# Kernel tuning notes

Hardware: AMD Instinct MI355X
Metric: run time of the kernel (lower is better)

Reference implementation:

```python
import jax, jax.numpy as jnp
import numpy as np

B, C, N, H = 4, 256, 1024, 8
D = C            # per-head q/k dim (out_channels defaults to in_channels)
DV = C           # per-head value/output dim (y_out_channels defaults to out_channels)


def setup_inputs() -> dict:
    key = jax.random.key(0)
    ks = jax.random.split(key, 10)
    s = 0.02
    return {
        "x": jax.random.normal(ks[0], (B, C, N), jnp.float32),
        "y": jax.random.normal(ks[1], (B, C, N), jnp.float32),
        "Wq": jax.random.normal(ks[2], (H * D, C), jnp.float32) * s,
        "bq": jnp.zeros((H * D,), jnp.float32),
        "Wk": jax.random.normal(ks[3], (H * D, C), jnp.float32) * s,
        "bk": jnp.zeros((H * D,), jnp.float32),
        "Wv": jax.random.normal(ks[4], (H * DV, C), jnp.float32) * s,
        "bv": jnp.zeros((H * DV,), jnp.float32),
        "Wp": jax.random.normal(ks[5], (DV, C), jnp.float32) * s,  # projection, bias=False
        "gamma": jax.random.uniform(ks[6], (H, 1, 1, 1), jnp.float32) + 0.001,
    }


def _pconv(t, W, b):
    # 1x1 conv1d: (O,C) x (B,C,N) -> (B,O,N)
    out = jnp.einsum('oc,bcn->bon', W, t)
    return out if b is None else out + b[None, :, None]


def reference(x, y, Wq, bq, Wk, bk, Wv, bv, Wp, gamma):
    b_, _, n_ = x.shape
    h = gamma.shape[0]
    # Q/K/V projections, split channels into h heads (head-major chunks of D)
    q = _pconv(x, Wq, bq).reshape(b_, h, -1, n_)   # [B,H,D,N]
    k = _pconv(x, Wk, bk).reshape(b_, h, -1, n_)   # [B,H,D,N]
    v = _pconv(y, Wv, bv).reshape(b_, h, -1, n_)   # [B,H,DV,N]
    # energy[i,j] = sum_d q[d,i]*k[d,j]; softmax over keys j (no sqrt(d) scaling)
    attn = jax.nn.softmax(jnp.einsum('bhdn,bhdm->bhnm', q, k), axis=-1)
    out = jnp.einsum('bhdm,bhnm->bhdn', v, attn)   # [B,H,DV,N]
    # residual branch: y projected to DV channels (1x1 conv, no bias)
    yp = jnp.einsum('oc,bcn->bon', Wp, y)          # [B,DV,N]
    g = gamma.reshape(1, h, 1, 1)
    out = (g * out + yp[:, None, :, :]) / (1.0 + g)
    # concat heads along channel dim (head-major), matching split_cat(out,1,0,2)
    return out.reshape(b_, -1, n_)                 # [B,H*DV,N]
```

## Files before the change

### kernel.cpp

```cpp
#include <hip/hip_runtime.h>

#define Bb 4
#define Cc 256
#define Nn 1024
#define Hh 8
#define Oo 2048

typedef __attribute__((ext_vector_type(8))) short bf16x8;
typedef __attribute__((ext_vector_type(4))) float f32x4;

__device__ __forceinline__ short f2bf(float f) {
  unsigned u = __builtin_bit_cast(unsigned, f);
  unsigned r = u + 0x7FFFu + ((u >> 16) & 1u);
  return (short)(r >> 16);
}
__device__ __forceinline__ f32x4 mfma16(bf16x8 a, bf16x8 b, f32x4 c) {
  return __builtin_amdgcn_mfma_f32_16x16x32_bf16(a, b, c, 0, 0, 0);
}
__device__ __forceinline__ void gl_lds16(const void* g, void* l) {
  __builtin_amdgcn_global_load_lds(
      (const __attribute__((address_space(1))) void*)g,
      (__attribute__((address_space(3))) void*)l, 16, 0, 0);
}

__device__ __forceinline__ void stage_row512(const char* gbase, char* lds,
                                             int wave, int lane) {
#pragma unroll
  for (int i = 0; i < 8; i++) {
    int off = (wave * 8 + i) * 1024;
    int L = off + lane * 16;
    int r = L >> 9;
    int c = ((L >> 4) & 31) ^ (r & 7);
    gl_lds16(gbase + r * 512 + c * 16, lds + off);
  }
}
__device__ __forceinline__ void stage_v(const char* Vg, char* lds, int k0,
                                        int wave, int lane) {
#pragma unroll
  for (int i = 0; i < 8; i++) {
    int off = (wave * 8 + i) * 1024;
    int L = off + lane * 16;
    int r = L >> 7;
    int c = ((L >> 4) & 7) ^ (r & 7);
    gl_lds16(Vg + (size_t)r * 2048 + k0 * 2 + c * 16, lds + off);
  }
}

__global__ __launch_bounds__(256) void k_transpose(
    const float* __restrict__ x, const float* __restrict__ y,
    short* __restrict__ xT, short* __restrict__ yT,
    const float* __restrict__ Wq, const float* __restrict__ Wk,
    const float* __restrict__ Wv, const float* __restrict__ Wp,
    short* __restrict__ dWq, short* __restrict__ dWk, short* __restrict__ dWv,
    short* __restrict__ dWp) {
  {
    const int NW = Oo * Cc;
    int lin = blockIdx.x + 16 * (blockIdx.y + 4 * blockIdx.z);
    for (int i = (lin * 256 + threadIdx.x) * 4; i < 3 * NW + Cc * Cc;
         i += 512 * 256 * 4) {
      const float* src;
      short* dst;
      int off;
      if (i < NW) {
        src = Wq; dst = dWq; off = i;
      } else if (i < 2 * NW) {
        src = Wk; dst = dWk; off = i - NW;
      } else if (i < 3 * NW) {
        src = Wv; dst = dWv; off = i - 2 * NW;
      } else {
        src = Wp; dst = dWp; off = i - 3 * NW;
      }
      float4 v = *(const float4*)(src + off);
      short4 o;
      o.x = f2bf(v.x);
      o.y = f2bf(v.y);
      o.z = f2bf(v.z);
      o.w = f2bf(v.w);
      *(short4*)(dst + off) = o;
    }
  }
  int bz = blockIdx.z;
  int b = bz >> 1;
  const float* src = (bz & 1) ? y : x;
  short* dst = (bz & 1) ? yT : xT;
  src += (size_t)b * Cc * Nn;
  dst += (size_t)b * Nn * Cc;
  __shared__ short tile[64][68];
  int n0 = blockIdx.x * 64, c0 = blockIdx.y * 64;
  int t = threadIdx.x;
#pragma unroll
  for (int i = 0; i < 4; i++) {
    int idx = t + i * 256;
    int cc = idx >> 4, ng = idx & 15;
    float4 v = *(const float4*)(src + (size_t)(c0 + cc) * Nn + n0 + ng * 4);
    short4 o;
    o.x = f2bf(v.x);
    o.y = f2bf(v.y);
    o.z = f2bf(v.z);
    o.w = f2bf(v.w);
    *(short4*)&tile[cc][ng * 4] = o;
  }
  __syncthreads();
#pragma unroll
  for (int i = 0; i < 4; i++) {
    int idx = t + i * 256;
    int nn = idx >> 4, c4 = idx & 15;
    short4 o;
    o.x = tile[c4 * 4 + 0][nn];
    o.y = tile[c4 * 4 + 1][nn];
    o.z = tile[c4 * 4 + 2][nn];
    o.w = tile[c4 * 4 + 3][nn];
    *(short4*)(dst + (size_t)(n0 + nn) * Cc + c0 + c4 * 4) = o;
  }
}

__global__ __launch_bounds__(256, 4) void k_proj(
    const short* __restrict__ xT, const short* __restrict__ yT,
    const short* __restrict__ Wqb, const float* __restrict__ bq,
    const short* __restrict__ Wkb, const float* __restrict__ bk,
    const short* __restrict__ Wvb, const float* __restrict__ bv,
    const short* __restrict__ Wpb, short* __restrict__ Qt,
    short* __restrict__ Kt, short* __restrict__ Vv, float* __restrict__ yp) {
  int b = blockIdx.z, n0 = blockIdx.x * 64;
  int yb = blockIdx.y;
  int path = yb >> 5;
  int o0 = (yb & 31) * 64;
  const short* W = path == 0 ? Wqb : path == 1 ? Wkb : path == 2 ? Wvb : Wpb;
  bool dataStaged = path >= 2;
  int wave = threadIdx.x >> 6, lane = threadIdx.x & 63;
  int quad = lane >> 4, l16 = lane & 15;
  int sw = l16 & 7;
  __shared__ short Ws[64 * 256];

  const char* stage_src =
      dataStaged ? (const char*)(yT + (size_t)b * Nn * Cc + (size_t)n0 * Cc)
                 : (const char*)(W + (size_t)o0 * Cc);
  stage_row512(stage_src, (char*)Ws, wave, lane);

  const short* aptr =
      dataStaged
          ? W + (size_t)(o0 + wave * 16 + l16) * Cc + quad * 8
          : xT + (size_t)b * Nn * Cc + (size_t)(n0 + wave * 16 + l16) * Cc +
                quad * 8;
  bf16x8 areg[8];
#pragma unroll
  for (int ks = 0; ks < 8; ks++) areg[ks] = *(const bf16x8*)(aptr + ks * 32);

  f32x4 acc[4];
#pragma unroll
  for (int j = 0; j < 4; j++) acc[j] = f32x4{0.f, 0.f, 0.f, 0.f};
  __syncthreads();
#pragma unroll
  for (int ks = 0; ks < 8; ks++) {
#pragma unroll
    for (int cj = 0; cj < 4; cj++) {
      int off = (cj * 16 + l16) * 512 + (((ks * 4 + quad) ^ sw) << 4);
      bf16x8 wf = *(const bf16x8*)((const char*)Ws + off);
      if (dataStaged)
        acc[cj] = mfma16(areg[ks], wf, acc[cj]);
      else
        acc[cj] = mfma16(wf, areg[ks], acc[cj]);
    }
  }
  if (path < 2) {
    short* Od = path == 0 ? Qt : Kt;
    const float* bias = path == 0 ? bq : bk;
#pragma unroll
    for (int cj = 0; cj < 4; cj++) {
      int obase = o0 + cj * 16 + quad * 4;
      int h = obase >> 8, d = obase & 255;
      int n = n0 + wave * 16 + l16;
      float4 vb = *(const float4*)(bias + obase);
      size_t idx = (((size_t)(b * Hh + h) * Nn) + n) * 256 + d;
      short4 o;
      o.x = f2bf(acc[cj][0] + vb.x);
      o.y = f2bf(acc[cj][1] + vb.y);
      o.z = f2bf(acc[cj][2] + vb.z);
      o.w = f2bf(acc[cj][3] + vb.w);
      *(short4*)(Od + idx) = o;
    }
  } else {
#pragma unroll
    for (int cj = 0; cj < 4; cj++) {
      int n = n0 + cj * 16 + l16;
#pragma unroll
      for (int r = 0; r < 4; r++) {
        int o = o0 + wave * 16 + quad * 4 + r;
        if (path == 3) {
          yp[((size_t)b * Cc + o) * Nn + n] = acc[cj][r];
        } else {
          float v = acc[cj][r] + bv[o];
          Vv[((size_t)b * Oo + o) * Nn + n] = f2bf(v);
        }
      }
    }
  }
}

__global__ __launch_bounds__(256) void k_attn(
    const short* __restrict__ Qt, const short* __restrict__ Kt,
    const short* __restrict__ Vv, const float* __restrict__ yp,
    const float* __restrict__ gamma, float* __restrict__ out) {
  int id = blockIdx.x;
  int bh = (id & 7) * 4 + (id >> 7);
  int q0 = ((id >> 3) & 15) * 64;
  int b = bh >> 3, h = bh & 7;
  int wave = threadIdx.x >> 6, lane = threadIdx.x & 63;
  int quad = lane >> 4, l16 = lane & 15;
  int sw = l16 & 7;
  const short* Qb = Qt + (size_t)bh * Nn * 256;
  const char* Kg = (const char*)(Kt + (size_t)bh * Nn * 256);
  const char* Vg = (const char*)(Vv + (size_t)bh * 256 * Nn);

  __shared__ short Klds[64 * 256];
  __shared__ short Vlds[256 * 64];
  __shared__ short plds[4][16][64];
  __shared__ float llds[64];

  bf16x8 qreg[8];
  {
    const short* qp = Qb + (size_t)(q0 + wave * 16 + l16) * 256 + quad * 8;
#pragma unroll
    for (int ks = 0; ks < 8; ks++) qreg[ks] = *(const bf16x8*)(qp + ks * 32);
  }
  f32x4 oacc[16];
#pragma unroll
  for (int j = 0; j < 16; j++) oacc[j] = f32x4{0.f, 0.f, 0.f, 0.f};
  float l_i[4] = {0.f, 0.f, 0.f, 0.f};

  stage_row512(Kg, (char*)Klds, wave, lane);
  stage_v(Vg, (char*)Vlds, 0, wave, lane);

  for (int kt = 0; kt < 16; kt++) {
    int k0 = kt * 64;
    __syncthreads();
    f32x4 sc[4];
#pragma unroll
    for (int j = 0; j < 4; j++) sc[j] = f32x4{0.f, 0.f, 0.f, 0.f};
#pragma unroll
    for (int ks = 0; ks < 8; ks++) {
#pragma unroll
      for (int cj = 0; cj < 4; cj++) {
        bf16x8 kb = *(const bf16x8*)((const char*)Klds +
                                     (cj * 16 + l16) * 512 +
                                     (((ks * 4 + quad) ^ sw) << 4));
        sc[cj] = mfma16(qreg[ks], kb, sc[cj]);
      }
    }
#pragma unroll
    for (int cj = 0; cj < 4; cj++) {
#pragma unroll
      for (int r = 0; r < 4; r++) {
        float p = __expf(sc[cj][r]);
        l_i[r] += p;
        int row = quad * 4 + r;
        plds[wave][row][(((cj * 2 + (l16 >> 3)) ^ (row & 7)) << 3) | sw] =
            f2bf(p);
      }
    }
    __syncthreads();
    if (kt < 15)
      stage_row512(Kg + (size_t)(k0 + 64) * 512, (char*)Klds, wave, lane);
    bf16x8 ap0[4], ap1[4];
#pragma unroll
    for (int qb = 0; qb < 4; qb++) {
      ap0[qb] = *(const bf16x8*)&plds[qb][l16][(quad ^ sw) << 3];
      ap1[qb] = *(const bf16x8*)&plds[qb][l16][((quad + 4) ^ sw) << 3];
    }
#pragma unroll
    for (int dj = 0; dj < 4; dj++) {
      const char* vrow = (const char*)Vlds + (wave * 64 + dj * 16 + l16) * 128;
      bf16x8 v0 = *(const bf16x8*)(vrow + ((quad ^ sw) << 4));
      bf16x8 v1 = *(const bf16x8*)(vrow + (((quad + 4) ^ sw) << 4));
#pragma unroll
      for (int qb = 0; qb < 4; qb++) {
        oacc[qb * 4 + dj] = mfma16(ap0[qb], v0, oacc[qb * 4 + dj]);
        oacc[qb * 4 + dj] = mfma16(ap1[qb], v1, oacc[qb * 4 + dj]);
      }
    }
    __syncthreads();
    if (kt < 15) stage_v(Vg, (char*)Vlds, k0 + 64, wave, lane);
  }
#pragma unroll
  for (int r = 0; r < 4; r++) {
    float v = l_i[r];
    v += __shfl_xor(v, 1);
    v += __shfl_xor(v, 2);
    v += __shfl_xor(v, 4);
    v += __shfl_xor(v, 8);
    l_i[r] = v;
  }
  if (l16 == 0) {
    f32x4 lv;
#pragma unroll
    for (int r = 0; r < 4; r++) lv[r] = l_i[r];
    *(f32x4*)&llds[wave * 16 + quad * 4] = lv;
  }
  __syncthreads();
  float gf = gamma[h];
  float sg = gf / (1.f + gf), sy = 1.f / (1.f + gf);
#pragma unroll
  for (int qb = 0; qb < 4; qb++) {
    f32x4 lv = *(const f32x4*)&llds[qb * 16 + quad * 4];
    int qq = q0 + qb * 16 + quad * 4;
#pragma unroll
    for (int dj = 0; dj < 4; dj++) {
      int dv = wave * 64 + dj * 16 + l16;
      const float* ypp = yp + ((size_t)b * 256 + dv) * Nn + qq;
      float* op = out + ((size_t)b * Oo + h * 256 + dv) * Nn + qq;
      float4 yv = *(const float4*)ypp;
      f32x4 oa = oacc[qb * 4 + dj];
      float4 ov;
      ov.x = sg * (oa[0] / lv[0]) + sy * yv.x;
      ov.y = sg * (oa[1] / lv[1]) + sy * yv.y;
      ov.z = sg * (oa[2] / lv[2]) + sy * yv.z;
      ov.w = sg * (oa[3] / lv[3]) + sy * yv.w;
      *(float4*)op = ov;
    }
  }
}

extern "C" void kernel_launch(void* const* d_in, const int* in_sizes, int n_in,
                              void* d_out, int out_size, void* d_ws,
                              size_t ws_size, hipStream_t stream) {
  const float* x = (const float*)d_in[0];
  const float* y = (const float*)d_in[1];
  const float* Wq = (const float*)d_in[2];
  const float* bq = (const float*)d_in[3];
  const float* Wk = (const float*)d_in[4];
  const float* bk = (const float*)d_in[5];
  const float* Wv = (const float*)d_in[6];
  const float* bv = (const float*)d_in[7];
  const float* Wp = (const float*)d_in[8];
  const float* gamma = (const float*)d_in[9];
  float* out = (float*)d_out;

  char* w = (char*)d_ws;
  short* Qt = (short*)(w + 0);
  short* Kt = (short*)(w + 16777216);
  short* Vv = (short*)(w + 33554432);
  short* xT = (short*)(w + 50331648);
  short* yT = (short*)(w + 52428800);
  float* yp = (float*)(w + 54525952);
  short* Wqb = (short*)(w + 58720256);
  short* Wkb = (short*)(w + 59768832);
  short* Wvb = (short*)(w + 60817408);
  short* Wpb = (short*)(w + 61865984);

  k_transpose<<<dim3(Nn / 64, Cc / 64, 2 * Bb), dim3(256), 0, stream>>>(
      x, y, xT, yT, Wq, Wk, Wv, Wp, Wqb, Wkb, Wvb, Wpb);
  k_proj<<<dim3(Nn / 64, 100, Bb), dim3(256), 0, stream>>>(
      xT, yT, Wqb, bq, Wkb, bk, Wvb, bv, Wpb, Qt, Kt, Vv, yp);
  k_attn<<<dim3(512), dim3(256), 0, stream>>>(Qt, Kt, Vv, yp, gamma, out);
}
```

Before: 189.5 us.

## Split attention block across eight waves partitioning keys and value dims

Result: no change. 192.2 us (+1.4%).

```diff
diff --git a/kernel.cpp b/kernel.cpp
--- a/kernel.cpp
+++ b/kernel.cpp
@@ -34,11 +34,22 @@
     gl_lds16(gbase + r * 512 + c * 16, lds + off);
   }
 }
-__device__ __forceinline__ void stage_v(const char* Vg, char* lds, int k0,
-                                        int wave, int lane) {
-#pragma unroll
-  for (int i = 0; i < 8; i++) {
-    int off = (wave * 8 + i) * 1024;
+__device__ __forceinline__ void stage_row512_8(const char* gbase, char* lds,
+                                               int wave, int lane) {
+#pragma unroll
+  for (int i = 0; i < 4; i++) {
+    int off = (wave * 4 + i) * 1024;
+    int L = off + lane * 16;
+    int r = L >> 9;
+    int c = ((L >> 4) & 31) ^ (r & 7);
+    gl_lds16(gbase + r * 512 + c * 16, lds + off);
+  }
+}
+__device__ __forceinline__ void stage_v8(const char* Vg, char* lds, int k0,
+                                         int wave, int lane) {
+#pragma unroll
+  for (int i = 0; i < 4; i++) {
+    int off = (wave * 4 + i) * 1024;
     int L = off + lane * 16;
     int r = L >> 7;
     int c = ((L >> 4) & 7) ^ (r & 7);
@@ -197,7 +208,7 @@
   }
 }
 
-__global__ __launch_bounds__(256) void k_attn(
+__global__ __launch_bounds__(512, 4) void k_attn(
     const short* __restrict__ Qt, const short* __restrict__ Kt,
     const short* __restrict__ Vv, const float* __restrict__ yp,
     const float* __restrict__ gamma, float* __restrict__ out) {
@@ -206,6 +217,7 @@
   int q0 = ((id >> 3) & 15) * 64;
   int b = bh >> 3, h = bh & 7;
   int wave = threadIdx.x >> 6, lane = threadIdx.x & 63;
+  int wq = wave >> 1, wk = wave & 1;
   int quad = lane >> 4, l16 = lane & 15;
   int sw = l16 & 7;
   const short* Qb = Qt + (size_t)bh * Nn * 256;
@@ -215,71 +227,71 @@
   __shared__ short Klds[64 * 256];
   __shared__ short Vlds[256 * 64];
   __shared__ short plds[4][16][64];
-  __shared__ float llds[64];
+  __shared__ float llds[2][64];
 
   bf16x8 qreg[8];
   {
-    const short* qp = Qb + (size_t)(q0 + wave * 16 + l16) * 256 + quad * 8;
+    const short* qp = Qb + (size_t)(q0 + wq * 16 + l16) * 256 + quad * 8;
 #pragma unroll
     for (int ks = 0; ks < 8; ks++) qreg[ks] = *(const bf16x8*)(qp + ks * 32);
   }
-  f32x4 oacc[16];
-#pragma unroll
-  for (int j = 0; j < 16; j++) oacc[j] = f32x4{0.f, 0.f, 0.f, 0.f};
+  f32x4 oacc[8];
+#pragma unroll
+  for (int j = 0; j < 8; j++) oacc[j] = f32x4{0.f, 0.f, 0.f, 0.f};
   float l_i[4] = {0.f, 0.f, 0.f, 0.f};
 
-  stage_row512(Kg, (char*)Klds, wave, lane);
-  stage_v(Vg, (char*)Vlds, 0, wave, lane);
+  stage_row512_8(Kg, (char*)Klds, wave, lane);
+  stage_v8(Vg, (char*)Vlds, 0, wave, lane);
 
   for (int kt = 0; kt < 16; kt++) {
     int k0 = kt * 64;
     __syncthreads();
-    f32x4 sc[4];
-#pragma unroll
-    for (int j = 0; j < 4; j++) sc[j] = f32x4{0.f, 0.f, 0.f, 0.f};
+    f32x4 sc[2];
+#pragma unroll
+    for (int j = 0; j < 2; j++) sc[j] = f32x4{0.f, 0.f, 0.f, 0.f};
 #pragma unroll
     for (int ks = 0; ks < 8; ks++) {
-#pragma unroll
-      for (int cj = 0; cj < 4; cj++) {
-        bf16x8 kb = *(const bf16x8*)((const char*)Klds +
-                                     (cj * 16 + l16) * 512 +
-                                     (((ks * 4 + quad) ^ sw) << 4));
-        sc[cj] = mfma16(qreg[ks], kb, sc[cj]);
-      }
-    }
-#pragma unroll
-    for (int cj = 0; cj < 4; cj++) {
+      bf16x8 kb0 = *(const bf16x8*)((const char*)Klds +
+                                    (wk * 32 + l16) * 512 +
+                                    (((ks * 4 + quad) ^ sw) << 4));
+      bf16x8 kb1 = *(const bf16x8*)((const char*)Klds +
+                                    (wk * 32 + 16 + l16) * 512 +
+                                    (((ks * 4 + quad) ^ sw) << 4));
+      sc[0] = mfma16(qreg[ks], kb0, sc[0]);
+      sc[1] = mfma16(qreg[ks], kb1, sc[1]);
+    }
+#pragma unroll
+    for (int cj = 0; cj < 2; cj++) {
 #pragma unroll
       for (int r = 0; r < 4; r++) {
         float p = __expf(sc[cj][r]);
         l_i[r] += p;
         int row = quad * 4 + r;
-        plds[wave][row][(((cj * 2 + (l16 >> 3)) ^ (row & 7)) << 3) | sw] =
-            f2bf(p);
+        int keyhi = wk * 4 + cj * 2 + (l16 >> 3);
+        plds[wq][row][((keyhi ^ (row & 7)) << 3) | sw] = f2bf(p);
       }
     }
     __syncthreads();
     if (kt < 15)
-      stage_row512(Kg + (size_t)(k0 + 64) * 512, (char*)Klds, wave, lane);
-    bf16x8 ap0[4], ap1[4];
-#pragma unroll
-    for (int qb = 0; qb < 4; qb++) {
-      ap0[qb] = *(const bf16x8*)&plds[qb][l16][(quad ^ sw) << 3];
-      ap1[qb] = *(const bf16x8*)&plds[qb][l16][((quad + 4) ^ sw) << 3];
-    }
-#pragma unroll
-    for (int dj = 0; dj < 4; dj++) {
-      const char* vrow = (const char*)Vlds + (wave * 64 + dj * 16 + l16) * 128;
-      bf16x8 v0 = *(const bf16x8*)(vrow + ((quad ^ sw) << 4));
-      bf16x8 v1 = *(const bf16x8*)(vrow + (((quad + 4) ^ sw) << 4));
-#pragma unroll
-      for (int qb = 0; qb < 4; qb++) {
-        oacc[qb * 4 + dj] = mfma16(ap0[qb], v0, oacc[qb * 4 + dj]);
-        oacc[qb * 4 + dj] = mfma16(ap1[qb], v1, oacc[qb * 4 + dj]);
+      stage_row512_8(Kg + (size_t)(k0 + 64) * 512, (char*)Klds, wave, lane);
+#pragma unroll
+    for (int c = 0; c < 2; c++) {
+      bf16x8 ap[4];
+#pragma unroll
+      for (int qb = 0; qb < 4; qb++)
+        ap[qb] = *(const bf16x8*)&plds[qb][l16][((c * 4 + quad) ^ sw) << 3];
+#pragma unroll
+      for (int dj = 0; dj < 2; dj++) {
+        const char* vrow =
+            (const char*)Vlds + (wave * 32 + dj * 16 + l16) * 128;
+        bf16x8 v = *(const bf16x8*)(vrow + (((c * 4 + quad) ^ sw) << 4));
+#pragma unroll
+        for (int qb = 0; qb < 4; qb++)
+          oacc[qb * 2 + dj] = mfma16(ap[qb], v, oacc[qb * 2 + dj]);
       }
     }
     __syncthreads();
-    if (kt < 15) stage_v(Vg, (char*)Vlds, k0 + 64, wave, lane);
+    if (kt < 15) stage_v8(Vg, (char*)Vlds, k0 + 64, wave, lane);
   }
 #pragma unroll
   for (int r = 0; r < 4; r++) {
@@ -294,27 +306,28 @@
     f32x4 lv;
 #pragma unroll
     for (int r = 0; r < 4; r++) lv[r] = l_i[r];
-    *(f32x4*)&llds[wave * 16 + quad * 4] = lv;
+    *(f32x4*)&llds[wk][wq * 16 + quad * 4] = lv;
   }
   __syncthreads();
   float gf = gamma[h];
   float sg = gf / (1.f + gf), sy = 1.f / (1.f + gf);
 #pragma unroll
   for (int qb = 0; qb < 4; qb++) {
-    f32x4 lv = *(const f32x4*)&llds[qb * 16 + quad * 4];
+    f32x4 lva = *(const f32x4*)&llds[0][qb * 16 + quad * 4];
+    f32x4 lvb = *(const f32x4*)&llds[1][qb * 16 + quad * 4];
     int qq = q0 + qb * 16 + quad * 4;
 #pragma unroll
-    for (int dj = 0; dj < 4; dj++) {
-      int dv = wave * 64 + dj * 16 + l16;
+    for (int dj = 0; dj < 2; dj++) {
+      int dv = wave * 32 + dj * 16 + l16;
       const float* ypp = yp + ((size_t)b * 256 + dv) * Nn + qq;
       float* op = out + ((size_t)b * Oo + h * 256 + dv) * Nn + qq;
       float4 yv = *(const float4*)ypp;
-      f32x4 oa = oacc[qb * 4 + dj];
+      f32x4 oa = oacc[qb * 2 + dj];
       float4 ov;
-      ov.x = sg * (oa[0] / lv[0]) + sy * yv.x;
-      ov.y = sg * (oa[1] / lv[1]) + sy * yv.y;
-      ov.z = sg * (oa[2] / lv[2]) + sy * yv.z;
-      ov.w = sg * (oa[3] / lv[3]) + sy * yv.w;
+      ov.x = sg * (oa[0] / (lva[0] + lvb[0])) + sy * yv.x;
+      ov.y = sg * (oa[1] / (lva[1] + lvb[1])) + sy * yv.y;
+      ov.z = sg * (oa[2] / (lva[2] + lvb[2])) + sy * yv.z;
+      ov.w = sg * (oa[3] / (lva[3] + lvb[3])) + sy * yv.w;
       *(float4*)op = ov;
     }
   }
@@ -351,5 +364,5 @@
       x, y, xT, yT, Wq, Wk, Wv, Wp, Wqb, Wkb, Wvb, Wpb);
   k_proj<<<dim3(Nn / 64, 100, Bb), dim3(256), 0, stream>>>(
       xT, yT, Wqb, bq, Wkb, bk, Wvb, bv, Wpb, Qt, Kt, Vv, yp);
-  k_attn<<<dim3(512), dim3(256), 0, stream>>>(Qt, Kt, Vv, yp, gamma, out);
-}
+  k_attn<<<dim3(512), dim3(512), 0, stream>>>(Qt, Kt, Vv, yp, gamma, out);
+}
```

## Stage activation tile once per block and loop over four weight chunks

Applied to the files above, without the earlier changes.

After: 221.7 us. +17.0%, slower.

```diff
diff --git a/kernel.cpp b/kernel.cpp
--- a/kernel.cpp
+++ b/kernel.cpp
@@ -114,7 +114,7 @@
   }
 }
 
-__global__ __launch_bounds__(256, 4) void k_proj(
+__global__ __launch_bounds__(256, 4) void k_proj2(
     const short* __restrict__ xT, const short* __restrict__ yT,
     const short* __restrict__ Wqb, const float* __restrict__ bq,
     const short* __restrict__ Wkb, const float* __restrict__ bk,
@@ -123,74 +123,83 @@
     short* __restrict__ Kt, short* __restrict__ Vv, float* __restrict__ yp) {
   int b = blockIdx.z, n0 = blockIdx.x * 64;
   int yb = blockIdx.y;
-  int path = yb >> 5;
-  int o0 = (yb & 31) * 64;
+  int path = yb >> 3;
+  int obase0 = (yb & 7) * 256;
   const short* W = path == 0 ? Wqb : path == 1 ? Wkb : path == 2 ? Wvb : Wpb;
-  bool dataStaged = path >= 2;
+  const short* data = path < 2 ? xT : yT;
   int wave = threadIdx.x >> 6, lane = threadIdx.x & 63;
   int quad = lane >> 4, l16 = lane & 15;
   int sw = l16 & 7;
   __shared__ short Ws[64 * 256];
 
-  const char* stage_src =
-      dataStaged ? (const char*)(yT + (size_t)b * Nn * Cc + (size_t)n0 * Cc)
-                 : (const char*)(W + (size_t)o0 * Cc);
-  stage_row512(stage_src, (char*)Ws, wave, lane);
-
-  const short* aptr =
-      dataStaged
-          ? W + (size_t)(o0 + wave * 16 + l16) * Cc + quad * 8
-          : xT + (size_t)b * Nn * Cc + (size_t)(n0 + wave * 16 + l16) * Cc +
-                quad * 8;
-  bf16x8 areg[8];
-#pragma unroll
-  for (int ks = 0; ks < 8; ks++) areg[ks] = *(const bf16x8*)(aptr + ks * 32);
-
-  f32x4 acc[4];
-#pragma unroll
-  for (int j = 0; j < 4; j++) acc[j] = f32x4{0.f, 0.f, 0.f, 0.f};
+  stage_row512((const char*)(data + (size_t)b * Nn * Cc + (size_t)n0 * Cc),
+               (char*)Ws, wave, lane);
   __syncthreads();
-#pragma unroll
-  for (int ks = 0; ks < 8; ks++) {
-#pragma unroll
-    for (int cj = 0; cj < 4; cj++) {
-      int off = (cj * 16 + l16) * 512 + (((ks * 4 + quad) ^ sw) << 4);
-      bf16x8 wf = *(const bf16x8*)((const char*)Ws + off);
-      if (dataStaged)
-        acc[cj] = mfma16(areg[ks], wf, acc[cj]);
-      else
-        acc[cj] = mfma16(wf, areg[ks], acc[cj]);
-    }
-  }
-  if (path < 2) {
-    short* Od = path == 0 ? Qt : Kt;
-    const float* bias = path == 0 ? bq : bk;
-#pragma unroll
-    for (int cj = 0; cj < 4; cj++) {
-      int obase = o0 + cj * 16 + quad * 4;
-      int h = obase >> 8, d = obase & 255;
-      int n = n0 + wave * 16 + l16;
-      float4 vb = *(const float4*)(bias + obase);
-      size_t idx = (((size_t)(b * Hh + h) * Nn) + n) * 256 + d;
-      short4 o;
-      o.x = f2bf(acc[cj][0] + vb.x);
-      o.y = f2bf(acc[cj][1] + vb.y);
-      o.z = f2bf(acc[cj][2] + vb.z);
-      o.w = f2bf(acc[cj][3] + vb.w);
-      *(short4*)(Od + idx) = o;
-    }
-  } else {
-#pragma unroll
-    for (int cj = 0; cj < 4; cj++) {
-      int n = n0 + cj * 16 + l16;
-#pragma unroll
-      for (int r = 0; r < 4; r++) {
-        int o = o0 + wave * 16 + quad * 4 + r;
-        if (path == 3) {
-          yp[((size_t)b * Cc + o) * Nn + n] = acc[cj][r];
-        } else {
-          float v = acc[cj][r] + bv[o];
-          Vv[((size_t)b * Oo + o) * Nn + n] = f2bf(v);
+
+#pragma unroll
+  for (int j = 0; j < 4; j++) {
+    int o0p = obase0 + j * 64;
+    const short* aptr = W + (size_t)(o0p + wave * 16 + l16) * Cc + quad * 8;
+    bf16x8 areg[8];
+#pragma unroll
+    for (int ks = 0; ks < 8; ks++) areg[ks] = *(const bf16x8*)(aptr + ks * 32);
+
+    f32x4 acc[4];
+#pragma unroll
+    for (int c = 0; c < 4; c++) acc[c] = f32x4{0.f, 0.f, 0.f, 0.f};
+#pragma unroll
+    for (int ks = 0; ks < 8; ks++) {
+#pragma unroll
+      for (int cj = 0; cj < 4; cj++) {
+        bf16x8 bb = *(const bf16x8*)((const char*)Ws + (cj * 16 + l16) * 512 +
+                                     (((ks * 4 + quad) ^ sw) << 4));
+        if (path < 2)
+          acc[cj] = mfma16(areg[ks], bb, acc[cj]);
+        else
+          acc[cj] = mfma16(bb, areg[ks], acc[cj]);
+      }
+    }
+    if (path < 2) {
+      short* Od = path == 0 ? Qt : Kt;
+      const float* bias = path == 0 ? bq : bk;
+      int ob = o0p + wave * 16 + quad * 4;
+      int h = ob >> 8, d = ob & 255;
+      float4 vb = *(const float4*)(bias + ob);
+#pragma unroll
+      for (int cj = 0; cj < 4; cj++) {
+        int n = n0 + cj * 16 + l16;
+        size_t idx = (((size_t)(b * Hh + h) * Nn) + n) * 256 + d;
+        short4 o;
+        o.x = f2bf(acc[cj][0] + vb.x);
+        o.y = f2bf(acc[cj][1] + vb.y);
+        o.z = f2bf(acc[cj][2] + vb.z);
+        o.w = f2bf(acc[cj][3] + vb.w);
+        *(short4*)(Od + idx) = o;
+      }
+    } else {
+      int o = o0p + wave * 16 + l16;
+      if (path == 3) {
+#pragma unroll
+        for (int cj = 0; cj < 4; cj++) {
+          int nb = n0 + cj * 16 + quad * 4;
+          float4 ov;
+          ov.x = acc[cj][0];
+          ov.y = acc[cj][1];
+          ov.z = acc[cj][2];
+          ov.w = acc[cj][3];
+          *(float4*)(yp + ((size_t)b * Cc + o) * Nn + nb) = ov;
+        }
+      } else {
+        float vbv = bv[o];
+#pragma unroll
+        for (int cj = 0; cj < 4; cj++) {
+          int nb = n0 + cj * 16 + quad * 4;
+          short4 ov;
+          ov.x = f2bf(acc[cj][0] + vbv);
+          ov.y = f2bf(acc[cj][1] + vbv);
+          ov.z = f2bf(acc[cj][2] + vbv);
+          ov.w = f2bf(acc[cj][3] + vbv);
+          *(short4*)(Vv + ((size_t)b * Oo + o) * Nn + nb) = ov;
         }
       }
     }
@@ -349,7 +358,7 @@
 
   k_transpose<<<dim3(Nn / 64, Cc / 64, 2 * Bb), dim3(256), 0, stream>>>(
       x, y, xT, yT, Wq, Wk, Wv, Wp, Wqb, Wkb, Wvb, Wpb);
-  k_proj<<<dim3(Nn / 64, 100, Bb), dim3(256), 0, stream>>>(
+  k_proj2<<<dim3(Nn / 64, 25, Bb), dim3(256), 0, stream>>>(
       xT, yT, Wqb, bq, Wkb, bk, Wvb, bv, Wpb, Qt, Kt, Vv, yp);
   k_attn<<<dim3(512), dim3(256), 0, stream>>>(Qt, Kt, Vv, yp, gamma, out);
 }
```
